# Optimization experiments

Measured on AMD Instinct MI355X. Metric: run time of the kernel, lower is better.

Reference implementation:

```python
import jax, jax.numpy as jnp
import numpy as np

B, C, N, K = 8, 256, 4096, 16

def setup_inputs() -> dict:
    key = jax.random.key(0)
    k1, k2, k3 = jax.random.split(key, 3)
    x = jax.random.normal(k1, (B, C, N, 1), dtype=jnp.float32)
    edge_index = jax.random.randint(k2, (2, B, N, K), 0, N, dtype=jnp.int64)
    eps = jnp.zeros((1,), dtype=jnp.float32)
    W = jax.random.normal(k3, (C, C), dtype=jnp.float32) * (1.0 / np.sqrt(C))
    b = jnp.zeros((C,), dtype=jnp.float32)
    return {"x": x, "edge_index": edge_index, "eps": eps, "W": W, "b": b}

def reference(x, edge_index, eps, W, b):
    # x: [B, C, N, 1]; edge_index: [2, B, N, K]
    idx = edge_index[0]                                  # [B, N, K] neighbor ids
    x_sq = x[..., 0]                                     # [B, C, N]
    # batched_index_select: gather neighbor features -> [B, C, N, K]
    gath = jnp.take_along_axis(
        x_sq, idx.reshape(B, 1, N * K).astype(jnp.int32), axis=2
    ).reshape(B, C, N, K)
    x_j = jnp.sum(gath, axis=-1, keepdims=True)          # [B, C, N, 1]
    h = (1.0 + eps[0]) * x + x_j                         # GIN update
    # BasicConv: 1x1 Conv2d + bias + ReLU
    out = jnp.einsum('oc,bcnk->bonk', W, h) + b[None, :, None, None]
    return jax.nn.relu(out)
```

## Files before the change

kernel.cpp:

```cpp
#include <hip/hip_runtime.h>
#include <hip/hip_bf16.h>
#include <stdint.h>

#define BB 8
#define CC 256
#define NN 4096
#define KK 16

typedef float f32x4 __attribute__((ext_vector_type(4)));
typedef short bf16x8 __attribute__((ext_vector_type(8)));

__device__ __forceinline__ ushort f2bf(float f) {
  union { float f; uint32_t u; } v; v.f = f;
  uint32_t r = v.u + 0x7FFFu + ((v.u >> 16) & 1u);
  return (ushort)(r >> 16);
}
__device__ __forceinline__ float bf2f(ushort h) {
  union { uint32_t u; float f; } v; v.u = ((uint32_t)h) << 16;
  return v.f;
}

__global__ __launch_bounds__(256) void k_transpose(
    const float* __restrict__ x, ushort* __restrict__ xT)
{
  __shared__ float tile[64][68];
  const int b  = blockIdx.z;
  const int c0 = blockIdx.y * 64;
  const int n0 = blockIdx.x * 64;
  const int t  = threadIdx.x;
  {
    const int r  = t >> 2;
    const int cs = (t & 3) * 16;
    const float* xp = x + ((size_t)b * CC + c0 + r) * NN + n0 + cs;
    #pragma unroll
    for (int i = 0; i < 4; ++i) {
      float4 v = *(const float4*)(xp + i * 4);
      *(float4*)&tile[r][cs + i * 4] = v;
    }
  }
  __syncthreads();
  const int nl = t >> 2;
  const int cl = (t & 3) * 16;
  union { ushort s[16]; uint4 q[2]; } pk;
  #pragma unroll
  for (int i = 0; i < 16; ++i) pk.s[i] = f2bf(tile[cl + i][nl]);
  uint4* dst = (uint4*)(xT + ((size_t)b * NN + n0 + nl) * CC + c0 + cl);
  dst[0] = pk.q[0];
  dst[1] = pk.q[1];
}

__global__ __launch_bounds__(256) void k_gather(
    const ushort* __restrict__ xT, const int* __restrict__ edge0,
    const float* __restrict__ eps, ushort* __restrict__ hT)
{
  const int b    = blockIdx.y;
  const int n0   = blockIdx.x * 16;
  const int t    = threadIdx.x;
  const int wave = t >> 6, lane = t & 63;
  const float epsv = 1.0f + eps[0];
  const int c4 = lane * 4;
  const ushort* xb = xT + (size_t)b * NN * CC;
  for (int i = 0; i < 4; ++i) {
    const int n = n0 + wave * 4 + i;
    ushort4 sv = *(const ushort4*)(xb + (size_t)n * CC + c4);
    float a0 = bf2f(sv.x) * epsv;
    float a1 = bf2f(sv.y) * epsv;
    float a2 = bf2f(sv.z) * epsv;
    float a3 = bf2f(sv.w) * epsv;
    const int* ep = edge0 + ((size_t)b * NN + n) * KK;
    #pragma unroll
    for (int k = 0; k < KK; ++k) {
      const int j = ep[k];
      ushort4 g = *(const ushort4*)(xb + (size_t)j * CC + c4);
      a0 += bf2f(g.x); a1 += bf2f(g.y); a2 += bf2f(g.z); a3 += bf2f(g.w);
    }
    ushort4 o;
    o.x = f2bf(a0); o.y = f2bf(a1); o.z = f2bf(a2); o.w = f2bf(a3);
    *(ushort4*)(hT + ((size_t)b * NN + n) * CC + c4) = o;
  }
}

__global__ __launch_bounds__(256) void k_gemm(
    const ushort* __restrict__ hT, const float* __restrict__ W,
    const float* __restrict__ bias, float* __restrict__ out)
{
  __shared__ ushort Wl[64][264];
  const int b  = blockIdx.z;
  const int o0 = blockIdx.y * 64;
  const int nb = blockIdx.x * 256;
  const int t  = threadIdx.x;
  const int wave = t >> 6, lane = t & 63;

  {
    const int r  = t >> 2;
    const int cs = (t & 3) * 64;
    const float* wp = W + (size_t)(o0 + r) * CC + cs;
    #pragma unroll
    for (int i = 0; i < 16; ++i) {
      float4 w4 = *(const float4*)(wp + i * 4);
      ushort4 h4;
      h4.x = f2bf(w4.x); h4.y = f2bf(w4.y); h4.z = f2bf(w4.z); h4.w = f2bf(w4.w);
      *(ushort4*)&Wl[r][cs + i * 4] = h4;
    }
  }
  __syncthreads();

  f32x4 acc[4][4];
  #pragma unroll
  for (int m = 0; m < 4; ++m)
    #pragma unroll
    for (int nn = 0; nn < 4; ++nn) acc[m][nn] = (f32x4){0.f, 0.f, 0.f, 0.f};

  const int lrow = lane & 15;
  const int kgrp = lane >> 4;
  const int nsub = nb + wave * 64;
  const ushort* hb = hT + (size_t)b * NN * CC;

  #pragma unroll
  for (int kc = 0; kc < 8; ++kc) {
    const int c0 = kc * 32;
    bf16x8 afr[4], bfr[4];
    #pragma unroll
    for (int m = 0; m < 4; ++m) {
      const ushort* ap = &Wl[m * 16 + lrow][c0 + kgrp * 8];
      afr[m] = *(const bf16x8*)ap;
    }
    #pragma unroll
    for (int nn = 0; nn < 4; ++nn) {
      const ushort* bp = hb + (size_t)(nsub + nn * 16 + lrow) * CC + c0 + kgrp * 8;
      bfr[nn] = *(const bf16x8*)bp;
    }
    #pragma unroll
    for (int m = 0; m < 4; ++m)
      #pragma unroll
      for (int nn = 0; nn < 4; ++nn)
        acc[m][nn] = __builtin_amdgcn_mfma_f32_16x16x32_bf16(
            afr[m], bfr[nn], acc[m][nn], 0, 0, 0);
  }

  #pragma unroll
  for (int m = 0; m < 4; ++m) {
    #pragma unroll
    for (int r = 0; r < 4; ++r) {
      const int o  = o0 + m * 16 + kgrp * 4 + r;
      const float bv = bias[o];
      #pragma unroll
      for (int nn = 0; nn < 4; ++nn) {
        const int n = nsub + nn * 16 + lrow;
        float v = acc[m][nn][r] + bv;
        v = v > 0.f ? v : 0.f;
        out[((size_t)b * CC + o) * NN + n] = v;
      }
    }
  }
}

extern "C" void kernel_launch(void* const* d_in, const int* in_sizes, int n_in,
                              void* d_out, int out_size, void* d_ws, size_t ws_size,
                              hipStream_t stream) {
  const float* x    = (const float*)d_in[0];
  const int*   edge = (const int*)d_in[1];
  const float* eps  = (const float*)d_in[2];
  const float* W    = (const float*)d_in[3];
  const float* bias = (const float*)d_in[4];
  float* out = (float*)d_out;

  ushort* xT = (ushort*)d_ws;
  ushort* hT = xT + (size_t)BB * NN * CC;

  dim3 g0(NN / 64, CC / 64, BB);
  k_transpose<<<g0, 256, 0, stream>>>(x, xT);

  dim3 g1(NN / 16, BB);
  k_gather<<<g1, 256, 0, stream>>>(xT, edge, eps, hT);

  dim3 g2(NN / 256, CC / 64, BB);
  k_gemm<<<g2, 256, 0, stream>>>(hT, W, bias, out);
}
```

Measured before the change: 145.0 us.

## Fuse neighbor gather with 1x1 conv GEMM via LDS-staged aggregated features

Merges the gather/aggregate kernel and the GEMM kernel, so each block aggregates 32 nodes into shared memory and immediately multiplies them by W in MFMA. This drops the global round trip of the bf16 hT buffer and one launch. W is pre-converted once per call into a fragment-friendly bf16 layout that is read straight from global memory. Edge indices are now loaded as int4 vectors, and batch is interleaved in the block index. In exchange, every block re-reads all of W (256x256) from cache, and the GEMM tile per block is smaller.

```diff
diff --git a/kernel.cpp b/kernel.cpp
--- a/kernel.cpp
+++ b/kernel.cpp
@@ -1,11 +1,11 @@
 #include <hip/hip_runtime.h>
-#include <hip/hip_bf16.h>
 #include <stdint.h>
 
 #define BB 8
 #define CC 256
 #define NN 4096
 #define KK 16
+#define NT 32
 
 typedef float f32x4 __attribute__((ext_vector_type(4)));
 typedef short bf16x8 __attribute__((ext_vector_type(8)));
@@ -49,91 +49,82 @@
   dst[1] = pk.q[1];
 }
 
-__global__ __launch_bounds__(256) void k_gather(
+__global__ __launch_bounds__(256) void k_wconv(
+    const float* __restrict__ W, ushort* __restrict__ Wfrag)
+{
+  const int t  = threadIdx.x;
+  const int o  = blockIdx.x * 4 + (t >> 6);
+  const int k0 = (t & 63) * 4;
+  float4 v = *(const float4*)(W + (size_t)o * CC + k0);
+  ushort4 h;
+  h.x = f2bf(v.x); h.y = f2bf(v.y); h.z = f2bf(v.z); h.w = f2bf(v.w);
+  const int kc = k0 >> 5, ks = k0 & 31;
+  *(ushort4*)(Wfrag + ((size_t)(kc * CC + o)) * 32 + ks) = h;
+}
+
+__global__ __launch_bounds__(256) void k_fused(
     const ushort* __restrict__ xT, const int* __restrict__ edge0,
-    const float* __restrict__ eps, ushort* __restrict__ hT)
+    const float* __restrict__ eps, const ushort* __restrict__ Wfrag,
+    const float* __restrict__ bias, float* __restrict__ out)
 {
-  const int b    = blockIdx.y;
-  const int n0   = blockIdx.x * 16;
+  __shared__ ushort hLds[NT][264];
+  const int bid = blockIdx.x;
+  const int b   = bid & 7;
+  const int n0  = (bid >> 3) * NT;
   const int t    = threadIdx.x;
   const int wave = t >> 6, lane = t & 63;
   const float epsv = 1.0f + eps[0];
+  const ushort* xb = xT + (size_t)b * NN * CC;
   const int c4 = lane * 4;
-  const ushort* xb = xT + (size_t)b * NN * CC;
-  for (int i = 0; i < 4; ++i) {
-    const int n = n0 + wave * 4 + i;
+
+  for (int i = 0; i < NT / 4; ++i) {
+    const int nl = wave * (NT / 4) + i;
+    const int n  = n0 + nl;
     ushort4 sv = *(const ushort4*)(xb + (size_t)n * CC + c4);
     float a0 = bf2f(sv.x) * epsv;
     float a1 = bf2f(sv.y) * epsv;
     float a2 = bf2f(sv.z) * epsv;
     float a3 = bf2f(sv.w) * epsv;
-    const int* ep = edge0 + ((size_t)b * NN + n) * KK;
+    const int4* epv = (const int4*)(edge0 + ((size_t)b * NN + n) * KK);
+    int4 e0 = epv[0], e1 = epv[1], e2 = epv[2], e3 = epv[3];
+    const int js[16] = {e0.x, e0.y, e0.z, e0.w, e1.x, e1.y, e1.z, e1.w,
+                        e2.x, e2.y, e2.z, e2.w, e3.x, e3.y, e3.z, e3.w};
     #pragma unroll
     for (int k = 0; k < KK; ++k) {
-      const int j = ep[k];
-      ushort4 g = *(const ushort4*)(xb + (size_t)j * CC + c4);
+      ushort4 g = *(const ushort4*)(xb + (size_t)js[k] * CC + c4);
       a0 += bf2f(g.x); a1 += bf2f(g.y); a2 += bf2f(g.z); a3 += bf2f(g.w);
     }
-    ushort4 o;
-    o.x = f2bf(a0); o.y = f2bf(a1); o.z = f2bf(a2); o.w = f2bf(a3);
-    *(ushort4*)(hT + ((size_t)b * NN + n) * CC + c4) = o;
-  }
-}
-
-__global__ __launch_bounds__(256) void k_gemm(
-    const ushort* __restrict__ hT, const float* __restrict__ W,
-    const float* __restrict__ bias, float* __restrict__ out)
-{
-  __shared__ ushort Wl[64][264];
-  const int b  = blockIdx.z;
-  const int o0 = blockIdx.y * 64;
-  const int nb = blockIdx.x * 256;
-  const int t  = threadIdx.x;
-  const int wave = t >> 6, lane = t & 63;
-
-  {
-    const int r  = t >> 2;
-    const int cs = (t & 3) * 64;
-    const float* wp = W + (size_t)(o0 + r) * CC + cs;
-    #pragma unroll
-    for (int i = 0; i < 16; ++i) {
-      float4 w4 = *(const float4*)(wp + i * 4);
-      ushort4 h4;
-      h4.x = f2bf(w4.x); h4.y = f2bf(w4.y); h4.z = f2bf(w4.z); h4.w = f2bf(w4.w);
-      *(ushort4*)&Wl[r][cs + i * 4] = h4;
-    }
+    ushort4 o4;
+    o4.x = f2bf(a0); o4.y = f2bf(a1); o4.z = f2bf(a2); o4.w = f2bf(a3);
+    *(ushort4*)&hLds[nl][c4] = o4;
   }
   __syncthreads();
 
-  f32x4 acc[4][4];
+  f32x4 acc[4][NT / 16];
   #pragma unroll
   for (int m = 0; m < 4; ++m)
     #pragma unroll
-    for (int nn = 0; nn < 4; ++nn) acc[m][nn] = (f32x4){0.f, 0.f, 0.f, 0.f};
+    for (int nn = 0; nn < NT / 16; ++nn) acc[m][nn] = (f32x4){0.f, 0.f, 0.f, 0.f};
 
   const int lrow = lane & 15;
   const int kgrp = lane >> 4;
-  const int nsub = nb + wave * 64;
-  const ushort* hb = hT + (size_t)b * NN * CC;
+  const int o0   = wave * 64;
 
   #pragma unroll
   for (int kc = 0; kc < 8; ++kc) {
-    const int c0 = kc * 32;
-    bf16x8 afr[4], bfr[4];
+    const int cs = kgrp * 8;
+    bf16x8 afr[4], bfr[NT / 16];
     #pragma unroll
-    for (int m = 0; m < 4; ++m) {
-      const ushort* ap = &Wl[m * 16 + lrow][c0 + kgrp * 8];
-      afr[m] = *(const bf16x8*)ap;
-    }
+    for (int m = 0; m < 4; ++m)
+      afr[m] = *(const bf16x8*)(Wfrag +
+          ((size_t)(kc * CC + o0 + m * 16 + lrow)) * 32 + cs);
     #pragma unroll
-    for (int nn = 0; nn < 4; ++nn) {
-      const ushort* bp = hb + (size_t)(nsub + nn * 16 + lrow) * CC + c0 + kgrp * 8;
-      bfr[nn] = *(const bf16x8*)bp;
-    }
+    for (int nn = 0; nn < NT / 16; ++nn)
+      bfr[nn] = *(const bf16x8*)&hLds[nn * 16 + lrow][kc * 32 + cs];
     #pragma unroll
     for (int m = 0; m < 4; ++m)
       #pragma unroll
-      for (int nn = 0; nn < 4; ++nn)
+      for (int nn = 0; nn < NT / 16; ++nn)
         acc[m][nn] = __builtin_amdgcn_mfma_f32_16x16x32_bf16(
             afr[m], bfr[nn], acc[m][nn], 0, 0, 0);
   }
@@ -145,8 +136,8 @@
       const int o  = o0 + m * 16 + kgrp * 4 + r;
       const float bv = bias[o];
       #pragma unroll
-      for (int nn = 0; nn < 4; ++nn) {
-        const int n = nsub + nn * 16 + lrow;
+      for (int nn = 0; nn < NT / 16; ++nn) {
+        const int n = n0 + nn * 16 + lrow;
         float v = acc[m][nn][r] + bv;
         v = v > 0.f ? v : 0.f;
         out[((size_t)b * CC + o) * NN + n] = v;
@@ -165,15 +156,13 @@
   const float* bias = (const float*)d_in[4];
   float* out = (float*)d_out;
 
-  ushort* xT = (ushort*)d_ws;
-  ushort* hT = xT + (size_t)BB * NN * CC;
+  ushort* xT    = (ushort*)d_ws;
+  ushort* Wfrag = xT + (size_t)BB * NN * CC;
 
   dim3 g0(NN / 64, CC / 64, BB);
   k_transpose<<<g0, 256, 0, stream>>>(x, xT);
 
-  dim3 g1(NN / 16, BB);
-  k_gather<<<g1, 256, 0, stream>>>(xT, edge, eps, hT);
+  k_wconv<<<CC / 4, 256, 0, stream>>>(W, Wfrag);
 
-  dim3 g2(NN / 256, CC / 64, BB);
-  k_gemm<<<g2, 256, 0, stream>>>(hT, W, bias, out);
+  k_fused<<<BB * (NN / NT), 256, 0, stream>>>(xT, edge, eps, Wfrag, bias, out);
 }
```

Result: faster. 128.0 us (-11.7%).
